# Kernel optimization log

Hardware: AMD Instinct MI355X
Metric: run time of the kernel (lower is better)

Reference implementation:

```python
import jax, jax.numpy as jnp
import numpy as np

K, PMAX, NUM_PTS = 20000, 30, 5
GEO_DIM, PE_DIM = 256, 32
C_OUT = GEO_DIM - PE_DIM  # 224
NUM_FREQS = 8


def setup_inputs() -> dict:
    key = jax.random.key(0)
    k = jax.random.split(key, 6)
    geoms = jax.random.normal(k[0], (K, PMAX, 2), dtype=jnp.float32) * 8.0  # ego BEV meters
    lengths = jax.random.randint(k[1], (K,), 2, PMAX + 1)                   # valid points per polyline
    w1 = jax.random.normal(k[2], (C_OUT // 2, 2, 3), jnp.float32) * 0.2
    b1 = jax.random.normal(k[3], (C_OUT // 2,), jnp.float32) * 0.02
    w2 = jax.random.normal(k[4], (C_OUT, C_OUT // 2, 3), jnp.float32) * 0.05
    b2 = jax.random.normal(k[5], (C_OUT,), jnp.float32) * 0.02
    gamma = jnp.ones((C_OUT,), jnp.float32)
    beta = jnp.zeros((C_OUT,), jnp.float32)
    return {"geoms": geoms, "lengths": lengths, "w1": w1, "b1": b1,
            "w2": w2, "b2": b2, "gamma": gamma, "beta": beta,
            "roi_w": 60, "roi_h": 30}


def _resample_one(coords, L):
    # coords: [PMAX,2] padded polyline; L: scalar int (>=2 valid points)
    diffs = coords[1:] - coords[:-1]                                  # [PMAX-1,2]
    sq = jnp.sum(diffs * diffs, axis=1)
    mask = (jnp.arange(PMAX - 1) < (L - 1)).astype(coords.dtype)      # valid segments
    seg = jnp.where(sq > 0, jnp.sqrt(jnp.where(sq > 0, sq, 1.0)), 0.0) * mask
    cum = jnp.concatenate([jnp.zeros((1,), coords.dtype), jnp.cumsum(seg)])  # [PMAX]
    total = cum[-1]
    targets = jnp.linspace(0.0, 1.0, NUM_PTS, dtype=coords.dtype) * total
    idx = jnp.clip(jnp.searchsorted(cum, targets, side='left'), 1, L - 1)
    t = (targets - cum[idx - 1]) / (seg[idx - 1] + 1e-8)
    pts = coords[idx - 1] + t[:, None] * diffs[idx - 1]               # [NUM_PTS,2]
    degen = total < 1e-6
    return jnp.where(degen, jnp.broadcast_to(coords[0], pts.shape), pts)


def _conv1d(x, w, b):
    # x: [K,C,5]; w: [O,C,3]; 'same' padding 1
    y = jax.lax.conv_general_dilated(x, w, (1,), ((1, 1),),
                                     dimension_numbers=('NCH', 'OIH', 'NCH'))
    return y + b[None, :, None]


def reference(geoms, lengths, w1, b1, w2, b2, gamma, beta, roi_w, roi_h):
    resampled = jax.vmap(_resample_one)(geoms, lengths)               # [K,5,2]
    roi_half = jnp.array([roi_w / 2.0, roi_h / 2.0], jnp.float32)
    roi_full = jnp.array([float(roi_w), float(roi_h)], jnp.float32)
    coords = (resampled + roi_half) / roi_full                        # [K,5,2] in [0,1]
    # sinusoidal PE: per coord dim [sin(x*2^f*pi) x8 | cos x8] -> flatten to 32
    freqs = (2.0 ** jnp.arange(NUM_FREQS, dtype=jnp.float32)) * np.float32(np.pi)
    xf = coords[..., None] * freqs                                    # [K,5,2,8]
    pe = jnp.concatenate([jnp.sin(xf), jnp.cos(xf)], axis=-1).reshape(-1, NUM_PTS, PE_DIM)
    x = coords.transpose(0, 2, 1)                                     # [K,2,5]
    x = jax.nn.relu(_conv1d(x, w1, b1))                               # [K,112,5]
    x = jax.nn.relu(_conv1d(x, w2, b2))                               # [K,224,5]
    x = x.transpose(0, 2, 1)                                          # [K,5,224]
    mu = jnp.mean(x, axis=-1, keepdims=True)
    var = jnp.mean((x - mu) ** 2, axis=-1, keepdims=True)
    x = (x - mu) * jax.lax.rsqrt(var + 1e-5) * gamma + beta
    geo_feats = jnp.concatenate([pe, x], axis=-1)                     # [K,5,256]
    return geo_feats, coords
```

## Files before the change

kernel.cpp:

```cpp
#include <hip/hip_runtime.h>
#include <math.h>

#define K_POLY   20000
#define PMAX     30
#define NUM_PTS  5
#define C_MID    112
#define C_OUT    224
#define PE_DIM   32
#define GEO_DIM  256
#define M_ROWS   (K_POLY*NUM_PTS)

#define ROWS_B   64
#define NPOLY_T  14
#define NTILES   14
#define KSTEPS   11
#define WP_ELEMS (KSTEPS*NTILES*64*8)
#define A_SLOTS  (NPOLY_T*7 + 1)

typedef __attribute__((ext_vector_type(8))) short short8;
typedef __attribute__((ext_vector_type(4))) float f32x4;

__device__ inline unsigned short f2bf(float f) {
    union { float f; unsigned u; } v; v.f = f;
    return (unsigned short)((v.u + 0x7fffu + ((v.u >> 16) & 1u)) >> 16);
}

__global__ void pack_w2(const float* __restrict__ w2, unsigned short* __restrict__ Wp) {
    int i = blockIdx.x * 256 + threadIdx.x;
    if (i >= WP_ELEMS) return;
    int j    = i & 7;
    int lane = (i >> 3) & 63;
    int grp  = i >> 9;
    int nt   = grp % NTILES;
    int ks   = grp / NTILES;
    int k    = ks * 32 + (lane >> 4) * 8 + j;
    int n    = nt * 16 + (lane & 15);
    float v = 0.f;
    if (k < 336) {
        int dk = k / C_MID, c = k - dk * C_MID;
        v = w2[(n * C_MID + c) * 3 + dk];
    }
    Wp[i] = f2bf(v);
}

__global__ __launch_bounds__(256, 4) void geo_fused(
    const float* __restrict__ geoms, const int* __restrict__ lengths,
    const float* __restrict__ w1, const float* __restrict__ b1,
    const float* __restrict__ b2, const float* __restrict__ gamma,
    const float* __restrict__ beta,
    const int* __restrict__ roi_w, const int* __restrict__ roi_h,
    const unsigned short* __restrict__ Wp,
    float* __restrict__ out)
{
    __shared__ __align__(16) unsigned short s_A[A_SLOTS * C_MID];
    __shared__ float s_geo[NPOLY_T][PMAX][2];
    __shared__ float s_cum[NPOLY_T][PMAX];
    __shared__ float s_seg[NPOLY_T][PMAX - 1];
    __shared__ float s_pts[NPOLY_T][NUM_PTS][2];
    __shared__ float s_w1[C_MID * 6];
    __shared__ float s_b1[C_MID];
    __shared__ int   s_len[NPOLY_T];

    const int t  = threadIdx.x;
    const int r0 = blockIdx.x * ROWS_B;
    const int pb = r0 / NUM_PTS;
    const int npoly = min(NPOLY_T, K_POLY - pb);

    {
        uint4* za = (uint4*)s_A;
        for (int i = t; i < (A_SLOTS * C_MID) / 8; i += 256) za[i] = uint4{0u, 0u, 0u, 0u};
    }
    {
        const float* src = geoms + (size_t)pb * (PMAX * 2);
        float* dst = &s_geo[0][0][0];
        for (int i = t; i < npoly * PMAX * 2; i += 256) dst[i] = src[i];
        if (t < npoly) s_len[t] = lengths[pb + t];
        for (int i = t; i < C_MID * 6; i += 256) s_w1[i] = w1[i];
        if (t < C_MID) s_b1[t] = b1[t];
    }
    __syncthreads();

    if (t < npoly) {
        int L = s_len[t];
        float cum = 0.f;
        s_cum[t][0] = 0.f;
        for (int i = 0; i < PMAX - 1; ++i) {
            float seg = 0.f;
            if (i < L - 1) {
                float dx = s_geo[t][i + 1][0] - s_geo[t][i][0];
                float dy = s_geo[t][i + 1][1] - s_geo[t][i][1];
                float sq = dx * dx + dy * dy;
                seg = (sq > 0.f) ? sqrtf(sq) : 0.f;
            }
            s_seg[t][i] = seg;
            cum += seg;
            s_cum[t][i + 1] = cum;
        }
    }
    __syncthreads();

    const float roiw  = (float)roi_w[0], roih = (float)roi_h[0];
    const float halfx = roiw * 0.5f, halfy = roih * 0.5f;
    if (t < npoly * NUM_PTS) {
        int poly = t / NUM_PTS, j = t % NUM_PTS;
        int L = s_len[poly];
        float total = s_cum[poly][PMAX - 1];
        float px, py;
        if (total < 1e-6f) {
            px = s_geo[poly][0][0];
            py = s_geo[poly][0][1];
        } else {
            float target = total * (0.25f * (float)j);
            int idx = PMAX;
            for (int i = 0; i < PMAX; ++i) {
                if (s_cum[poly][i] >= target) { idx = i; break; }
            }
            idx = max(1, min(idx, L - 1));
            float tt = (target - s_cum[poly][idx - 1]) / (s_seg[poly][idx - 1] + 1e-8f);
            float x0 = s_geo[poly][idx - 1][0], y0 = s_geo[poly][idx - 1][1];
            px = x0 + tt * (s_geo[poly][idx][0] - x0);
            py = y0 + tt * (s_geo[poly][idx][1] - y0);
        }
        float cx = (px + halfx) / roiw;
        float cy = (py + halfy) / roih;
        s_pts[poly][j][0] = cx;
        s_pts[poly][j][1] = cy;
        float* co = out + (size_t)M_ROWS * GEO_DIM + ((size_t)(pb + poly) * NUM_PTS + j) * 2;
        co[0] = cx;
        co[1] = cy;
    }
    __syncthreads();

    for (int i = t; i < npoly * NUM_PTS * C_MID; i += 256) {
        int poly = i / (NUM_PTS * C_MID);
        int r = i % (NUM_PTS * C_MID);
        int p = r / C_MID;
        int c = r % C_MID;
        float acc = s_b1[c];
        const float* w = &s_w1[c * 6];
        #pragma unroll
        for (int ch = 0; ch < 2; ++ch) {
            #pragma unroll
            for (int dk = 0; dk < 3; ++dk) {
                int pp = p + dk - 1;
                float xv = (pp >= 0 && pp < NUM_PTS) ? s_pts[poly][pp][ch] : 0.f;
                acc += xv * w[ch * 3 + dk];
            }
        }
        s_A[(poly * 7 + p + 1) * C_MID + c] = f2bf(fmaxf(acc, 0.f));
    }
    __syncthreads();

    const int lane = t & 63;
    const int wave = t >> 6;
    const int quad = lane >> 4;
    const int m    = lane & 15;
    const int rw   = r0 + wave * 16;

    int rA = min(rw + m, M_ROWS - 1);
    int polyA = rA / NUM_PTS, pA = rA - polyA * NUM_PTS;
    const int abase = ((polyA - pb) * 7 + pA) * C_MID + quad * 8;

    f32x4 acc[NTILES];
    #pragma unroll
    for (int nt = 0; nt < NTILES; ++nt)
        #pragma unroll
        for (int i = 0; i < 4; ++i) acc[nt][i] = 0.f;

    const unsigned short* wl = Wp + lane * 8;
    #pragma unroll
    for (int ks = 0; ks < KSTEPS; ++ks) {
        short8 a = *(const short8*)(s_A + abase + ks * 32);
        #pragma unroll
        for (int nt = 0; nt < NTILES; ++nt) {
            short8 b = *(const short8*)(wl + ((ks * NTILES + nt) << 9));
            acc[nt] = __builtin_amdgcn_mfma_f32_16x16x32_bf16(a, b, acc[nt], 0, 0, 0);
        }
    }

    {
        const int col = lane & 31;
        const int d   = col >> 4;
        const int isc = (col >> 3) & 1;
        const int fr  = col & 7;
        const float pef = (float)(1 << fr) * 3.14159265358979323846f;
        #pragma unroll
        for (int it = 0; it < 8; ++it) {
            int r = rw + it * 2 + (lane >> 5);
            if (r < M_ROWS) {
                int lp = r / NUM_PTS - pb, j = r % NUM_PTS;
                float x = s_pts[lp][j][d];
                float arg = x * pef;
                float v = isc ? __cosf(arg) : __sinf(arg);
                out[(size_t)r * GEO_DIM + col] = v;
            }
        }
    }

    float bias[NTILES], g[NTILES], be[NTILES];
    #pragma unroll
    for (int nt = 0; nt < NTILES; ++nt) {
        int col = nt * 16 + m;
        bias[nt] = b2[col];
        g[nt]    = gamma[col];
        be[nt]   = beta[col];
    }
    #pragma unroll
    for (int nt = 0; nt < NTILES; ++nt)
        #pragma unroll
        for (int i = 0; i < 4; ++i)
            acc[nt][i] = fmaxf(acc[nt][i] + bias[nt], 0.f);

    #pragma unroll
    for (int i = 0; i < 4; ++i) {
        float s = 0.f, q = 0.f;
        #pragma unroll
        for (int nt = 0; nt < NTILES; ++nt) {
            float v = acc[nt][i];
            s += v;
            q += v * v;
        }
        #pragma unroll
        for (int mk = 8; mk >= 1; mk >>= 1) {
            s += __shfl_xor(s, mk, 64);
            q += __shfl_xor(q, mk, 64);
        }
        float mu  = s * (1.f / C_OUT);
        float var = fmaxf(q * (1.f / C_OUT) - mu * mu, 0.f);
        float rs  = rsqrtf(var + 1e-5f);

        int r = rw + quad * 4 + i;
        if (r < M_ROWS) {
            size_t ob = (size_t)r * GEO_DIM + PE_DIM + m;
            #pragma unroll
            for (int nt = 0; nt < NTILES; ++nt)
                out[ob + nt * 16] = (acc[nt][i] - mu) * rs * g[nt] + be[nt];
        }
    }
}

extern "C" void kernel_launch(void* const* d_in, const int* in_sizes, int n_in,
                              void* d_out, int out_size, void* d_ws, size_t ws_size,
                              hipStream_t stream) {
    const float* geoms   = (const float*)d_in[0];
    const int*   lengths = (const int*)d_in[1];
    const float* w1      = (const float*)d_in[2];
    const float* b1      = (const float*)d_in[3];
    const float* w2      = (const float*)d_in[4];
    const float* b2      = (const float*)d_in[5];
    const float* gamma   = (const float*)d_in[6];
    const float* beta    = (const float*)d_in[7];
    const int*   roi_w   = (const int*)d_in[8];
    const int*   roi_h   = (const int*)d_in[9];
    float* out = (float*)d_out;
    unsigned short* Wp = (unsigned short*)d_ws;

    hipLaunchKernelGGL(pack_w2, dim3((WP_ELEMS + 255) / 256), dim3(256), 0, stream, w2, Wp);
    hipLaunchKernelGGL(geo_fused, dim3((M_ROWS + ROWS_B - 1) / ROWS_B), dim3(256), 0, stream,
                       geoms, lengths, w1, b1, b2, gamma, beta, roi_w, roi_h, Wp, out);
}
```

Before: 194.6 us.

## Split into prep and GEMM kernels with LDS double-buffered weights

The fused kernel is split in two. A prep kernel packs w2 and resamples each polyline with one wavefront per polyline, using a shuffle prefix scan and ballot-based search, then writes conv1 bf16 activations into scratch space inside the output buffer. A second GEMM kernel has each wave handle two 16-row M tiles (30 rows), so every B fragment is reused twice. B is double-buffered in LDS via global_load_lds, and the A operand is prefetched from global memory. This cuts the global weight reads per row and serialises less per-block setup, at the cost of writing the intermediate activations to global memory and reading them back.

```diff
diff --git a/kernel.cpp b/kernel.cpp
--- a/kernel.cpp
+++ b/kernel.cpp
@@ -10,12 +10,20 @@
 #define GEO_DIM  256
 #define M_ROWS   (K_POLY*NUM_PTS)
 
-#define ROWS_B   64
-#define NPOLY_T  14
 #define NTILES   14
 #define KSTEPS   11
 #define WP_ELEMS (KSTEPS*NTILES*64*8)
-#define A_SLOTS  (NPOLY_T*7 + 1)
+#define NPACK_BLK ((WP_ELEMS+255)/256)
+#define POLY_PER_BLK 4
+#define NPREP_BLK ((K_POLY+POLY_PER_BLK-1)/POLY_PER_BLK)
+
+#define CHUNK_STRIDE 2560
+#define CHUNK_OFF    64
+
+#define ROWS_W   30
+#define WAVES_B  4
+#define NWAVES2  ((M_ROWS+ROWS_W-1)/ROWS_W)
+#define NBLK2    ((NWAVES2+WAVES_B-1)/WAVES_B)
 
 typedef __attribute__((ext_vector_type(8))) short short8;
 typedef __attribute__((ext_vector_type(4))) float f32x4;
@@ -25,218 +33,228 @@
     return (unsigned short)((v.u + 0x7fffu + ((v.u >> 16) & 1u)) >> 16);
 }
 
-__global__ void pack_w2(const float* __restrict__ w2, unsigned short* __restrict__ Wp) {
-    int i = blockIdx.x * 256 + threadIdx.x;
-    if (i >= WP_ELEMS) return;
-    int j    = i & 7;
-    int lane = (i >> 3) & 63;
-    int grp  = i >> 9;
-    int nt   = grp % NTILES;
-    int ks   = grp / NTILES;
-    int k    = ks * 32 + (lane >> 4) * 8 + j;
-    int n    = nt * 16 + (lane & 15);
-    float v = 0.f;
-    if (k < 336) {
-        int dk = k / C_MID, c = k - dk * C_MID;
-        v = w2[(n * C_MID + c) * 3 + dk];
-    }
-    Wp[i] = f2bf(v);
-}
-
-__global__ __launch_bounds__(256, 4) void geo_fused(
+#define GLDS(gp, lp) __builtin_amdgcn_global_load_lds( \
+    (const __attribute__((address_space(1))) void*)(gp), \
+    (__attribute__((address_space(3))) void*)(lp), 16, 0, 0)
+
+__global__ __launch_bounds__(256) void prep_pack(
     const float* __restrict__ geoms, const int* __restrict__ lengths,
     const float* __restrict__ w1, const float* __restrict__ b1,
+    const float* __restrict__ w2,
+    const int* __restrict__ roi_w, const int* __restrict__ roi_h,
+    unsigned short* __restrict__ Wp, float* __restrict__ out)
+{
+    if (blockIdx.x < NPACK_BLK) {
+        int i = blockIdx.x * 256 + threadIdx.x;
+        if (i < WP_ELEMS) {
+            int j    = i & 7;
+            int lane = (i >> 3) & 63;
+            int grp  = i >> 9;
+            int nt   = grp % NTILES;
+            int ks   = grp / NTILES;
+            int k    = ks * 32 + (lane >> 4) * 8 + j;
+            int n    = nt * 16 + (lane & 15);
+            float v = 0.f;
+            if (k < 336) {
+                int dk = k / C_MID, c = k - dk * C_MID;
+                v = w2[(n * C_MID + c) * 3 + dk];
+            }
+            Wp[i] = f2bf(v);
+        }
+        return;
+    }
+
+    const int poly = (blockIdx.x - NPACK_BLK) * POLY_PER_BLK + (threadIdx.x >> 6);
+    const int lane = threadIdx.x & 63;
+    if (poly >= K_POLY) return;
+
+    const float* gp = geoms + (size_t)poly * (PMAX * 2);
+    float px = 0.f, py = 0.f;
+    if (lane < PMAX) { float2 p = ((const float2*)gp)[lane]; px = p.x; py = p.y; }
+    const int L = lengths[poly];
+
+    float nx = __shfl(px, lane + 1);
+    float ny = __shfl(py, lane + 1);
+    float seg = 0.f;
+    if (lane < L - 1 && lane < PMAX - 1) {
+        float dx = nx - px, dy = ny - py;
+        float sq = dx * dx + dy * dy;
+        seg = (sq > 0.f) ? sqrtf(sq) : 0.f;
+    }
+    float incl = seg;
+    #pragma unroll
+    for (int d = 1; d < 32; d <<= 1) {
+        float v = __shfl_up(incl, d, 32);
+        if ((lane & 31) >= d) incl += v;
+    }
+    float cum = __shfl_up(incl, 1, 32);
+    if ((lane & 31) == 0) cum = 0.f;
+    const float total = __shfl(incl, PMAX - 2);
+
+    const float roiw = (float)roi_w[0], roih = (float)roi_h[0];
+    const float halfx = roiw * 0.5f, halfy = roih * 0.5f;
+    const bool degen = total < 1e-6f;
+    const float x0g = __shfl(px, 0), y0g = __shfl(py, 0);
+
+    float bxv[NUM_PTS], byv[NUM_PTS];
+    #pragma unroll
+    for (int j = 0; j < NUM_PTS; ++j) {
+        float tj = total * (0.25f * (float)j);
+        unsigned long long mlt = __ballot(lane < PMAX && cum < tj);
+        int idx = (int)__popcll(mlt);
+        idx = max(1, min(idx, L - 1));
+        float c1 = __shfl(cum, idx - 1);
+        float s1 = __shfl(seg, idx - 1);
+        float ax = __shfl(px, idx - 1), ay = __shfl(py, idx - 1);
+        float bx2 = __shfl(px, idx),    by2 = __shfl(py, idx);
+        float tt = (tj - c1) / (s1 + 1e-8f);
+        float fx = degen ? x0g : ax + tt * (bx2 - ax);
+        float fy = degen ? y0g : ay + tt * (by2 - ay);
+        bxv[j] = (fx + halfx) / roiw;
+        byv[j] = (fy + halfy) / roih;
+    }
+    if (lane == 0) {
+        float* co = out + (size_t)M_ROWS * GEO_DIM + (size_t)poly * (NUM_PTS * 2);
+        #pragma unroll
+        for (int j = 0; j < NUM_PTS; ++j) { co[2 * j] = bxv[j]; co[2 * j + 1] = byv[j]; }
+    }
+
+    unsigned short* chunk = (unsigned short*)out + (size_t)poly * CHUNK_STRIDE + CHUNK_OFF;
+    unsigned int* cz = (unsigned int*)chunk;
+    if (lane < 56) cz[lane] = 0u;
+    cz[336 + lane] = 0u;
+
+    #pragma unroll
+    for (int it = 0; it < 2; ++it) {
+        int c = it * 64 + lane;
+        if (c < C_MID) {
+            const float* w = w1 + c * 6;
+            float w0 = w[0], wa = w[1], wb = w[2], w3 = w[3], w4 = w[4], w5 = w[5];
+            float bb = b1[c];
+            #pragma unroll
+            for (int p = 0; p < NUM_PTS; ++p) {
+                float acc = bb + bxv[p] * wa + byv[p] * w4;
+                if (p > 0)           acc += bxv[p - 1] * w0 + byv[p - 1] * w3;
+                if (p < NUM_PTS - 1) acc += bxv[p + 1] * wb + byv[p + 1] * w5;
+                chunk[(p + 1) * C_MID + c] = f2bf(fmaxf(acc, 0.f));
+            }
+        }
+    }
+}
+
+__global__ __launch_bounds__(256, 3) void gemm2(
+    const unsigned short* __restrict__ Wp,
     const float* __restrict__ b2, const float* __restrict__ gamma,
-    const float* __restrict__ beta,
-    const int* __restrict__ roi_w, const int* __restrict__ roi_h,
-    const unsigned short* __restrict__ Wp,
-    float* __restrict__ out)
+    const float* __restrict__ beta, float* __restrict__ out)
 {
-    __shared__ __align__(16) unsigned short s_A[A_SLOTS * C_MID];
-    __shared__ float s_geo[NPOLY_T][PMAX][2];
-    __shared__ float s_cum[NPOLY_T][PMAX];
-    __shared__ float s_seg[NPOLY_T][PMAX - 1];
-    __shared__ float s_pts[NPOLY_T][NUM_PTS][2];
-    __shared__ float s_w1[C_MID * 6];
-    __shared__ float s_b1[C_MID];
-    __shared__ int   s_len[NPOLY_T];
-
-    const int t  = threadIdx.x;
-    const int r0 = blockIdx.x * ROWS_B;
-    const int pb = r0 / NUM_PTS;
-    const int npoly = min(NPOLY_T, K_POLY - pb);
+    __shared__ __align__(16) unsigned short s_B[2][NTILES * 512];
+
+    const int t = threadIdx.x, lane = t & 63, wave = t >> 6;
+    const int quad = lane >> 4, m = lane & 15;
+    const int rw = (blockIdx.x * WAVES_B + wave) * ROWS_W;
+
+    int r0 = min(rw + m, M_ROWS - 1);
+    int r1 = min(rw + 16 + m, M_ROWS - 1);
+    int poly0 = r0 / 5, p0 = r0 - poly0 * 5;
+    int poly1 = r1 / 5, p1 = r1 - poly1 * 5;
+    const unsigned short* A = (const unsigned short*)out;
+    const unsigned short* Ab0 = A + (size_t)poly0 * CHUNK_STRIDE + CHUNK_OFF + p0 * C_MID + quad * 8;
+    const unsigned short* Ab1 = A + (size_t)poly1 * CHUNK_STRIDE + CHUNK_OFF + p1 * C_MID + quad * 8;
+
+    f32x4 acc0[NTILES], acc1[NTILES];
+    #pragma unroll
+    for (int nt = 0; nt < NTILES; ++nt)
+        #pragma unroll
+        for (int i = 0; i < 4; ++i) { acc0[nt][i] = 0.f; acc1[nt][i] = 0.f; }
+
+    const char* WpB = (const char*)Wp;
+    #pragma unroll
+    for (int j = 0; j < 4; ++j) {
+        int sgi = j * WAVES_B + wave;
+        if (sgi < NTILES)
+            GLDS(WpB + sgi * 1024 + lane * 16, (char*)&s_B[0][0] + sgi * 1024);
+    }
+    short8 a0 = *(const short8*)Ab0;
+    short8 a1 = *(const short8*)Ab1;
+    __syncthreads();
+
+    int buf = 0;
+    for (int ks = 0; ks < KSTEPS; ++ks) {
+        short8 a0n = a0, a1n = a1;
+        if (ks < KSTEPS - 1) {
+            const char* src = WpB + (size_t)(ks + 1) * (NTILES * 1024);
+            #pragma unroll
+            for (int j = 0; j < 4; ++j) {
+                int sgi = j * WAVES_B + wave;
+                if (sgi < NTILES)
+                    GLDS(src + sgi * 1024 + lane * 16, (char*)&s_B[buf ^ 1][0] + sgi * 1024);
+            }
+            a0n = *(const short8*)(Ab0 + (ks + 1) * 32);
+            a1n = *(const short8*)(Ab1 + (ks + 1) * 32);
+        }
+        const unsigned short* bp = &s_B[buf][lane * 8];
+        #pragma unroll
+        for (int nt = 0; nt < NTILES; ++nt) {
+            short8 b = *(const short8*)(bp + nt * 512);
+            acc0[nt] = __builtin_amdgcn_mfma_f32_16x16x32_bf16(a0, b, acc0[nt], 0, 0, 0);
+            acc1[nt] = __builtin_amdgcn_mfma_f32_16x16x32_bf16(a1, b, acc1[nt], 0, 0, 0);
+        }
+        __syncthreads();
+        buf ^= 1; a0 = a0n; a1 = a1n;
+    }
 
     {
-        uint4* za = (uint4*)s_A;
-        for (int i = t; i < (A_SLOTS * C_MID) / 8; i += 256) za[i] = uint4{0u, 0u, 0u, 0u};
-    }
-    {
-        const float* src = geoms + (size_t)pb * (PMAX * 2);
-        float* dst = &s_geo[0][0][0];
-        for (int i = t; i < npoly * PMAX * 2; i += 256) dst[i] = src[i];
-        if (t < npoly) s_len[t] = lengths[pb + t];
-        for (int i = t; i < C_MID * 6; i += 256) s_w1[i] = w1[i];
-        if (t < C_MID) s_b1[t] = b1[t];
-    }
-    __syncthreads();
-
-    if (t < npoly) {
-        int L = s_len[t];
-        float cum = 0.f;
-        s_cum[t][0] = 0.f;
-        for (int i = 0; i < PMAX - 1; ++i) {
-            float seg = 0.f;
-            if (i < L - 1) {
-                float dx = s_geo[t][i + 1][0] - s_geo[t][i][0];
-                float dy = s_geo[t][i + 1][1] - s_geo[t][i][1];
-                float sq = dx * dx + dy * dy;
-                seg = (sq > 0.f) ? sqrtf(sq) : 0.f;
-            }
-            s_seg[t][i] = seg;
-            cum += seg;
-            s_cum[t][i + 1] = cum;
-        }
-    }
-    __syncthreads();
-
-    const float roiw  = (float)roi_w[0], roih = (float)roi_h[0];
-    const float halfx = roiw * 0.5f, halfy = roih * 0.5f;
-    if (t < npoly * NUM_PTS) {
-        int poly = t / NUM_PTS, j = t % NUM_PTS;
-        int L = s_len[poly];
-        float total = s_cum[poly][PMAX - 1];
-        float px, py;
-        if (total < 1e-6f) {
-            px = s_geo[poly][0][0];
-            py = s_geo[poly][0][1];
-        } else {
-            float target = total * (0.25f * (float)j);
-            int idx = PMAX;
-            for (int i = 0; i < PMAX; ++i) {
-                if (s_cum[poly][i] >= target) { idx = i; break; }
-            }
-            idx = max(1, min(idx, L - 1));
-            float tt = (target - s_cum[poly][idx - 1]) / (s_seg[poly][idx - 1] + 1e-8f);
-            float x0 = s_geo[poly][idx - 1][0], y0 = s_geo[poly][idx - 1][1];
-            px = x0 + tt * (s_geo[poly][idx][0] - x0);
-            py = y0 + tt * (s_geo[poly][idx][1] - y0);
-        }
-        float cx = (px + halfx) / roiw;
-        float cy = (py + halfy) / roih;
-        s_pts[poly][j][0] = cx;
-        s_pts[poly][j][1] = cy;
-        float* co = out + (size_t)M_ROWS * GEO_DIM + ((size_t)(pb + poly) * NUM_PTS + j) * 2;
-        co[0] = cx;
-        co[1] = cy;
-    }
-    __syncthreads();
-
-    for (int i = t; i < npoly * NUM_PTS * C_MID; i += 256) {
-        int poly = i / (NUM_PTS * C_MID);
-        int r = i % (NUM_PTS * C_MID);
-        int p = r / C_MID;
-        int c = r % C_MID;
-        float acc = s_b1[c];
-        const float* w = &s_w1[c * 6];
-        #pragma unroll
-        for (int ch = 0; ch < 2; ++ch) {
-            #pragma unroll
-            for (int dk = 0; dk < 3; ++dk) {
-                int pp = p + dk - 1;
-                float xv = (pp >= 0 && pp < NUM_PTS) ? s_pts[poly][pp][ch] : 0.f;
-                acc += xv * w[ch * 3 + dk];
-            }
-        }
-        s_A[(poly * 7 + p + 1) * C_MID + c] = f2bf(fmaxf(acc, 0.f));
-    }
-    __syncthreads();
-
-    const int lane = t & 63;
-    const int wave = t >> 6;
-    const int quad = lane >> 4;
-    const int m    = lane & 15;
-    const int rw   = r0 + wave * 16;
-
-    int rA = min(rw + m, M_ROWS - 1);
-    int polyA = rA / NUM_PTS, pA = rA - polyA * NUM_PTS;
-    const int abase = ((polyA - pb) * 7 + pA) * C_MID + quad * 8;
-
-    f32x4 acc[NTILES];
-    #pragma unroll
-    for (int nt = 0; nt < NTILES; ++nt)
-        #pragma unroll
-        for (int i = 0; i < 4; ++i) acc[nt][i] = 0.f;
-
-    const unsigned short* wl = Wp + lane * 8;
-    #pragma unroll
-    for (int ks = 0; ks < KSTEPS; ++ks) {
-        short8 a = *(const short8*)(s_A + abase + ks * 32);
-        #pragma unroll
-        for (int nt = 0; nt < NTILES; ++nt) {
-            short8 b = *(const short8*)(wl + ((ks * NTILES + nt) << 9));
-            acc[nt] = __builtin_amdgcn_mfma_f32_16x16x32_bf16(a, b, acc[nt], 0, 0, 0);
-        }
-    }
-
-    {
+        const float* cptr = out + (size_t)M_ROWS * GEO_DIM;
         const int col = lane & 31;
-        const int d   = col >> 4;
-        const int isc = (col >> 3) & 1;
-        const int fr  = col & 7;
+        const int d = col >> 4, isc = (col >> 3) & 1, fr = col & 7;
         const float pef = (float)(1 << fr) * 3.14159265358979323846f;
         #pragma unroll
-        for (int it = 0; it < 8; ++it) {
+        for (int it = 0; it < 15; ++it) {
             int r = rw + it * 2 + (lane >> 5);
             if (r < M_ROWS) {
-                int lp = r / NUM_PTS - pb, j = r % NUM_PTS;
-                float x = s_pts[lp][j][d];
+                float x = cptr[(size_t)r * 2 + d];
                 float arg = x * pef;
-                float v = isc ? __cosf(arg) : __sinf(arg);
-                out[(size_t)r * GEO_DIM + col] = v;
-            }
-        }
-    }
-
-    float bias[NTILES], g[NTILES], be[NTILES];
+                out[(size_t)r * GEO_DIM + col] = isc ? __cosf(arg) : __sinf(arg);
+            }
+        }
+    }
+
+    float bias[NTILES], gm[NTILES], bt[NTILES];
     #pragma unroll
     for (int nt = 0; nt < NTILES; ++nt) {
         int col = nt * 16 + m;
-        bias[nt] = b2[col];
-        g[nt]    = gamma[col];
-        be[nt]   = beta[col];
-    }
-    #pragma unroll
-    for (int nt = 0; nt < NTILES; ++nt)
-        #pragma unroll
-        for (int i = 0; i < 4; ++i)
-            acc[nt][i] = fmaxf(acc[nt][i] + bias[nt], 0.f);
-
-    #pragma unroll
-    for (int i = 0; i < 4; ++i) {
-        float s = 0.f, q = 0.f;
-        #pragma unroll
-        for (int nt = 0; nt < NTILES; ++nt) {
-            float v = acc[nt][i];
-            s += v;
-            q += v * v;
-        }
-        #pragma unroll
-        for (int mk = 8; mk >= 1; mk >>= 1) {
-            s += __shfl_xor(s, mk, 64);
-            q += __shfl_xor(q, mk, 64);
-        }
-        float mu  = s * (1.f / C_OUT);
-        float var = fmaxf(q * (1.f / C_OUT) - mu * mu, 0.f);
-        float rs  = rsqrtf(var + 1e-5f);
-
-        int r = rw + quad * 4 + i;
-        if (r < M_ROWS) {
-            size_t ob = (size_t)r * GEO_DIM + PE_DIM + m;
-            #pragma unroll
-            for (int nt = 0; nt < NTILES; ++nt)
-                out[ob + nt * 16] = (acc[nt][i] - mu) * rs * g[nt] + be[nt];
-        }
-    }
+        bias[nt] = b2[col]; gm[nt] = gamma[col]; bt[nt] = beta[col];
+    }
+
+    auto epilogue = [&](f32x4 (&acc)[NTILES], int g) {
+        #pragma unroll
+        for (int i = 0; i < 4; ++i) {
+            float s = 0.f, q = 0.f;
+            #pragma unroll
+            for (int nt = 0; nt < NTILES; ++nt) {
+                float v = fmaxf(acc[nt][i] + bias[nt], 0.f);
+                acc[nt][i] = v;
+                s += v; q += v * v;
+            }
+            #pragma unroll
+            for (int mk = 8; mk >= 1; mk >>= 1) {
+                s += __shfl_xor(s, mk, 64);
+                q += __shfl_xor(q, mk, 64);
+            }
+            float mu  = s * (1.f / C_OUT);
+            float var = fmaxf(q * (1.f / C_OUT) - mu * mu, 0.f);
+            float rs  = rsqrtf(var + 1e-5f);
+            int r = rw + g * 16 + quad * 4 + i;
+            if (r < M_ROWS && !(g == 1 && quad == 3 && i >= 2)) {
+                size_t ob = (size_t)r * GEO_DIM + PE_DIM + m;
+                #pragma unroll
+                for (int nt = 0; nt < NTILES; ++nt)
+                    out[ob + nt * 16] = (acc[nt][i] - mu) * rs * gm[nt] + bt[nt];
+            }
+        }
+    };
+    epilogue(acc0, 0);
+    epilogue(acc1, 1);
 }
 
 extern "C" void kernel_launch(void* const* d_in, const int* in_sizes, int n_in,
@@ -255,7 +273,7 @@
     float* out = (float*)d_out;
     unsigned short* Wp = (unsigned short*)d_ws;
 
-    hipLaunchKernelGGL(pack_w2, dim3((WP_ELEMS + 255) / 256), dim3(256), 0, stream, w2, Wp);
-    hipLaunchKernelGGL(geo_fused, dim3((M_ROWS + ROWS_B - 1) / ROWS_B), dim3(256), 0, stream,
-                       geoms, lengths, w1, b1, b2, gamma, beta, roi_w, roi_h, Wp, out);
-}
+    hipLaunchKernelGGL(prep_pack, dim3(NPACK_BLK + NPREP_BLK), dim3(256), 0, stream,
+                       geoms, lengths, w1, b1, w2, roi_w, roi_h, Wp, out);
+    hipLaunchKernelGGL(gemm2, dim3(NBLK2), dim3(256), 0, stream, Wp, b2, gamma, beta, out);
+}
```

Result: no change. 194.3 us (-0.2%).
